# Performance work log

Measured on AMD Instinct MI355X. Metric: run time of the kernel, lower is better.

Reference implementation:

```python
import jax, jax.numpy as jnp
import numpy as np

T, A = 4096, 4          # tokens, atoms per token
N = T * A               # flat atoms
QB, KB = 32, 128        # query block / key window (AF3 atom transformer)
S = N // QB             # number of query subsets
H, DK = 4, 32           # heads, key dim per head
NB = 3                  # transformer blocks
CA, CP, CT = 128, 16, 384

# clipped sliding key window centered on each 32-atom query block
KIDX = jnp.clip(jnp.arange(S)[:, None] * QB - (KB - QB) // 2 + jnp.arange(KB)[None, :], 0, N - 1)

PARAM_SHAPES = [('w_ref_pos', (3, CA)), ('w_ref_mask', (1, CA)), ('w_ref_element', (CA, CA)), ('w_ref_charge', (1, CA)), ('w_ref_atom_name', (256, CA)), ('w_s2p_row', (CA, CP)), ('w_s2p_col', (CA, CP)), ('w_pair_offsets', (3, CP)), ('w_pair_dist', (1, CP)), ('w_pair_mask', (1, CP)), ('w_pair_mlp1', (CP, CP)), ('w_pair_mlp2', (CP, CP)), ('w_pair_mlp3', (CP, CP)), ('w_pair_ln', (CP,)), ('w_pair_logits', (CP, NB * H)), ('aq_lnw', (NB, CA)), ('aq_gw', (NB, CA, CA)), ('aq_gb', (NB, CA)), ('aq_sw', (NB, CA, CA)), ('ak_lnw', (NB, CA)), ('ak_gw', (NB, CA, CA)), ('ak_gb', (NB, CA)), ('ak_sw', (NB, CA, CA)), ('wq', (NB, CA, CA)), ('bq', (NB, CA)), ('wk', (NB, CA, CA)), ('wv', (NB, CA, CA)), ('wg', (NB, CA, CA)), ('azi_w', (NB, CA, CA)), ('azi_cw', (NB, CA, CA)), ('azi_cb', (NB, CA)), ('t_lnw', (NB, CA)), ('t_gw', (NB, CA, CA)), ('t_gb', (NB, CA)), ('t_sw', (NB, CA, CA)), ('glu1', (NB, CA, 2 * CA)), ('glu2', (NB, CA, 2 * CA)), ('t_azi_w', (NB, 2 * CA, CA)), ('t_azi_cw', (NB, CA, CA)), ('t_azi_cb', (NB, CA)), ('w_project', (CA, CT))]


def _ln(x, w=None, eps=1e-5):
    mu = jnp.mean(x, -1, keepdims=True)
    var = jnp.var(x, -1, keepdims=True)
    xn = (x - mu) * jax.lax.rsqrt(var + eps)
    return xn * w if w is not None else xn


def _ada_ln(x, cond, lnw, gw, gb, sw):
    c = _ln(cond, lnw)
    return jax.nn.sigmoid(c @ gw + gb) * _ln(x) + c @ sw


def setup_inputs() -> dict:
    ks = iter(jax.random.split(jax.random.key(0), 64))
    d = {}
    d['positions'] = jax.random.normal(next(ks), (T, A, 3), jnp.float32) * 3.0
    d['mask'] = jnp.ones((T, A), jnp.float32)
    d['element'] = jax.random.randint(next(ks), (T, A), 0, 128, jnp.int32)
    d['charge'] = jax.random.normal(next(ks), (T, A), jnp.float32)
    d['atom_name_chars'] = jax.random.randint(next(ks), (T, A, 4), 0, 64, jnp.int32)
    d['ref_space_uid'] = jax.random.randint(next(ks), (T, A), 0, T, jnp.int32)
    for nm, shp in PARAM_SHAPES:
        if nm.endswith('lnw') or nm == 'w_pair_ln':
            d[nm] = jnp.ones(shp, jnp.float32)
        else:
            d[nm] = jax.random.normal(next(ks), shp, jnp.float32) * 0.02
    return d


def _forward(positions, mask, charge, w_ref_pos, w_ref_mask, w_ref_element, w_ref_charge, w_ref_atom_name, w_s2p_row, w_s2p_col, w_pair_offsets, w_pair_dist, w_pair_mask, w_pair_mlp1, w_pair_mlp2, w_pair_mlp3, w_pair_ln, w_pair_logits, aq_lnw, aq_gw, aq_gb, aq_sw, ak_lnw, ak_gw, ak_gb, ak_sw, wq, bq, wk, wv, wg, azi_w, azi_cw, azi_cb, t_lnw, t_gw, t_gb, t_sw, glu1, glu2, t_azi_w, t_azi_cw, t_azi_cb, w_project, element, atom_name_chars, ref_space_uid):
    dt = positions.dtype
    pos = positions.reshape(N, 3)
    m = mask.reshape(N, 1)
    # per_atom_cond
    el1h = jax.nn.one_hot(element.reshape(N), 128, dtype=dt)
    nm1h = jax.nn.one_hot(atom_name_chars.reshape(N, 4), 64, dtype=dt).reshape(N, 256)
    ch = jnp.arcsinh(charge.reshape(N, 1))
    act = pos @ w_ref_pos + m @ w_ref_mask + el1h @ w_ref_element + ch @ w_ref_charge + nm1h @ w_ref_atom_name
    act = act * m
    qsc = act.reshape(S, QB, CA)  # queries_single_cond
    # pair conditioning
    uid = ref_space_uid.reshape(N)
    q_uid, k_uid = uid.reshape(S, QB), uid[KIDX]
    q_pos, k_pos = pos.reshape(S, QB, 3), pos[KIDX]
    valid = (q_uid[:, :, None] == k_uid[:, None, :]).astype(dt)[..., None]  # [S,QB,KB,1]
    off = q_pos[:, :, None, :] - k_pos[:, None, :, :]  # [S,QB,KB,3]
    pair = (off @ w_pair_offsets) * valid
    sq = jnp.sum(off * off, -1, keepdims=True)
    pair = pair + ((1.0 / (1.0 + sq)) @ w_pair_dist) * valid
    ksc = act[KIDX]  # keys_single_cond [S,KB,CA]
    pair = pair + (jax.nn.relu(qsc) @ w_s2p_row)[:, :, None, :] + (jax.nn.relu(ksc) @ w_s2p_col)[:, None, :, :]
    pair = pair + valid @ w_pair_mask
    t = jax.nn.relu(pair) @ w_pair_mlp1
    t = jax.nn.relu(t) @ w_pair_mlp2
    t = jax.nn.relu(t) @ w_pair_mlp3
    pair = pair + t
    # pair logits for all blocks: [NB, S, H, QB, KB]
    pl = (_ln(pair, w_pair_ln) @ w_pair_logits).reshape(S, QB, KB, NB, H)
    pl = jnp.transpose(pl, (3, 0, 4, 1, 2))
    qact = qsc
    scale = DK ** -0.5
    for i in range(NB):
        kact = qact.reshape(N, CA)[KIDX]
        xq = _ada_ln(qact, qsc, aq_lnw[i], aq_gw[i], aq_gb[i], aq_sw[i])
        xk = _ada_ln(kact, ksc, ak_lnw[i], ak_gw[i], ak_gb[i], ak_sw[i])
        q = (xq @ wq[i] + bq[i]).reshape(S, QB, H, DK)
        k = (xk @ wk[i]).reshape(S, KB, H, DK)
        logits = jnp.einsum('sqhd,skhd->shqk', q * scale, k) + pl[i]
        aw = jax.nn.softmax(logits, axis=-1)
        v = (xk @ wv[i]).reshape(S, KB, H, DK)
        o = jnp.einsum('shqk,skhd->sqhd', aw, v).reshape(S, QB, CA)
        o = o * jax.nn.sigmoid(xq @ wg[i])
        o = (o @ azi_w[i]) * jax.nn.sigmoid(qsc @ azi_cw[i] + azi_cb[i])  # AdaptiveZeroInit
        qact = qact + o
        xt = _ada_ln(qact, qsc, t_lnw[i], t_gw[i], t_gb[i], t_sw[i])
        xt = jax.nn.silu(xt @ glu1[i]) * (xt @ glu2[i])  # SwiGLU
        xt = (xt @ t_azi_w[i]) * jax.nn.sigmoid(qsc @ t_azi_cw[i] + t_azi_cb[i])
        qact = qact + xt
    tok = jax.nn.relu(qact.reshape(T, A, CA) @ w_project)
    mm = mask[..., None]
    token_act = jnp.sum(tok * mm, -2) / jnp.maximum(jnp.sum(mm, -2), 1e-10)
    return token_act, qact, qsc, pair


def reference(positions, mask, element, charge, atom_name_chars, ref_space_uid, w_ref_pos, w_ref_mask, w_ref_element, w_ref_charge, w_ref_atom_name, w_s2p_row, w_s2p_col, w_pair_offsets, w_pair_dist, w_pair_mask, w_pair_mlp1, w_pair_mlp2, w_pair_mlp3, w_pair_ln, w_pair_logits, aq_lnw, aq_gw, aq_gb, aq_sw, ak_lnw, ak_gw, ak_gb, ak_sw, wq, bq, wk, wv, wg, azi_w, azi_cw, azi_cb, t_lnw, t_gw, t_gb, t_sw, glu1, glu2, t_azi_w, t_azi_cw, t_azi_cb, w_project):
    return _forward(positions, mask, charge, w_ref_pos, w_ref_mask, w_ref_element, w_ref_charge, w_ref_atom_name, w_s2p_row, w_s2p_col, w_pair_offsets, w_pair_dist, w_pair_mask, w_pair_mlp1, w_pair_mlp2, w_pair_mlp3, w_pair_ln, w_pair_logits, aq_lnw, aq_gw, aq_gb, aq_sw, ak_lnw, ak_gw, ak_gb, ak_sw, wq, bq, wk, wv, wg, azi_w, azi_cw, azi_cb, t_lnw, t_gw, t_gb, t_sw, glu1, glu2, t_azi_w, t_azi_cw, t_azi_cb, w_project, element, atom_name_chars, ref_space_uid)
```

## Files before the change

kernel.cpp:

```cpp
#include <hip/hip_runtime.h>
#include <math.h>

#define TT 4096
#define AA 4
#define NN 16384
#define QBQ 32
#define KBK 128
#define SS 512
#define HH 4
#define DKD 32
#define CAC 128
#define CPC 16
#define CTC 384

#define EPI_PLAIN 0
#define EPI_SIG   1
#define EPI_RELU  3

typedef __attribute__((ext_vector_type(8))) short bf16x8;
typedef __attribute__((ext_vector_type(4))) short s16x4;
typedef __attribute__((ext_vector_type(4))) float f32x4;

__device__ __forceinline__ float sig_(float x) { return 1.0f / (1.0f + __expf(-x)); }
__device__ __forceinline__ short f2bf(float f) {
    unsigned u = __float_as_uint(f);
    unsigned r = (u + 0x7FFFu + ((u >> 16) & 1u)) >> 16;
    return (short)r;
}
__device__ __forceinline__ float b2f(short s) {
    return __uint_as_float(((unsigned)(unsigned short)s) << 16);
}

struct PEnt { const float* src; const float* rs; short* dst; int K; int NC; };
struct PTab { PEnt e[49]; };

__global__ __launch_bounds__(256) void k_prep(PTab tab)
{
    const PEnt e = tab.e[blockIdx.y];
    const int ntx = e.NC >> 5, nty = e.K >> 5, nt = ntx * nty;
    __shared__ float sm[32][33];
    const int lx = threadIdx.x & 31, ly = threadIdx.x >> 5;
    for (int t = blockIdx.x; t < nt; t += gridDim.x) {
        const int ty = t / ntx, tx = t - ty * ntx;
        #pragma unroll
        for (int j = 0; j < 4; ++j) {
            const int k = ty * 32 + ly + j * 8;
            const int n = tx * 32 + lx;
            float v = e.src[(size_t)k * e.NC + n];
            if (e.rs) v *= e.rs[k];
            sm[ly + j * 8][lx] = v;
        }
        __syncthreads();
        #pragma unroll
        for (int j = 0; j < 4; ++j) {
            const int n = tx * 32 + ly + j * 8;
            const int k = ty * 32 + lx;
            e.dst[(size_t)n * e.K + k] = f2bf(sm[lx][ly + j * 8]);
        }
        __syncthreads();
    }
}

__global__ __launch_bounds__(128) void k_atom_cond(
    const float* __restrict__ pos, const float* __restrict__ msk,
    const int* __restrict__ elem, const float* __restrict__ chg,
    const int* __restrict__ chars,
    const float* __restrict__ w_pos, const float* __restrict__ w_msk,
    const float* __restrict__ w_elem, const float* __restrict__ w_chg,
    const float* __restrict__ w_name,
    const float* __restrict__ w_row, const float* __restrict__ w_col,
    float* __restrict__ qsc, float* __restrict__ qact,
    short* __restrict__ qsc_bf, short* __restrict__ qn_bf,
    float* __restrict__ rq, float* __restrict__ rk)
{
    const int n = blockIdx.x, c = threadIdx.x;
    const float p0 = pos[n*3+0], p1 = pos[n*3+1], p2 = pos[n*3+2];
    const float m = msk[n];
    const int   el = elem[n];
    const float ach = asinhf(chg[n]);
    const int c0 = chars[n*4+0], c1 = chars[n*4+1], c2 = chars[n*4+2], c3 = chars[n*4+3];

    float a = p0*w_pos[c] + p1*w_pos[CAC+c] + p2*w_pos[2*CAC+c]
            + m*w_msk[c] + w_elem[el*CAC+c] + ach*w_chg[c]
            + w_name[(c0      )*CAC+c] + w_name[( 64+c1)*CAC+c]
            + w_name[(128+c2)*CAC+c] + w_name[(192+c3)*CAC+c];
    a *= m;

    const size_t base = (size_t)n*CAC + c;
    qsc[base] = a; qact[base] = a; qsc_bf[base] = f2bf(a);

    __shared__ float red[128];
    __shared__ float sh[128];
    red[c] = a; __syncthreads();
    for (int off = 64; off > 0; off >>= 1) { if (c < off) red[c] += red[c+off]; __syncthreads(); }
    const float mu = red[0] * (1.0f/128.0f);
    __syncthreads();
    const float d = a - mu;
    red[c] = d*d; __syncthreads();
    for (int off = 64; off > 0; off >>= 1) { if (c < off) red[c] += red[c+off]; __syncthreads(); }
    const float var = red[0] * (1.0f/128.0f);
    qn_bf[base] = f2bf(d * rsqrtf(var + 1e-5f));
    __syncthreads();
    sh[c] = fmaxf(a, 0.0f);
    __syncthreads();
    if (c < 32) {
        const float* w = (c < 16) ? w_row : w_col;
        const int cc = c & 15;
        float acc = 0.0f;
        #pragma unroll 8
        for (int r = 0; r < 128; ++r) acc += sh[r] * w[r*CPC + cc];
        if (c < 16) rq[(size_t)n*CPC + cc] = acc;
        else        rk[(size_t)n*CPC + cc] = acc;
    }
}

__global__ __launch_bounds__(256) void k_pair(
    const float* __restrict__ pos, const int* __restrict__ uid,
    const float* __restrict__ rq, const float* __restrict__ rk,
    const float* __restrict__ w_ofs, const float* __restrict__ w_dist,
    const float* __restrict__ w_pm,
    const float* __restrict__ mlp1, const float* __restrict__ mlp2,
    const float* __restrict__ mlp3,
    const float* __restrict__ wln, const float* __restrict__ wpl,
    float* __restrict__ pair, short* __restrict__ plb)
{
    __shared__ float sm1[256], sm2[256], sm3[256], sofs[48], sdist[16], smask[16];
    __shared__ float swln[16], swpl[192];
    const int tid = threadIdx.x;
    sm1[tid] = mlp1[tid]; sm2[tid] = mlp2[tid]; sm3[tid] = mlp3[tid];
    if (tid < 48) sofs[tid] = w_ofs[tid];
    if (tid < 16) { sdist[tid] = w_dist[tid]; smask[tid] = w_pm[tid]; swln[tid] = wln[tid]; }
    if (tid < 192) swpl[tid] = wpl[tid];
    __syncthreads();

    const int gid = blockIdx.x*256 + tid;
    const int s = gid >> 12;
    const int rem = gid & 4095;
    const int q = rem >> 7, kk = rem & 127;
    const int n = s*QBQ + q;
    int kidx = s*QBQ - 48 + kk; kidx = max(0, min(NN-1, kidx));

    const float v = (uid[n] == uid[kidx]) ? 1.0f : 0.0f;
    const float o0 = pos[n*3+0]-pos[kidx*3+0];
    const float o1 = pos[n*3+1]-pos[kidx*3+1];
    const float o2 = pos[n*3+2]-pos[kidx*3+2];
    const float sq = o0*o0 + o1*o1 + o2*o2;
    const float inv = 1.0f/(1.0f + sq);

    const float* rqp = rq + (size_t)n*CPC;
    const float* rkp = rk + (size_t)kidx*CPC;

    float p[16], t1[16], t2[16];
    #pragma unroll
    for (int j = 0; j < 16; ++j)
        p[j] = v*(o0*sofs[j] + o1*sofs[16+j] + o2*sofs[32+j] + inv*sdist[j] + smask[j])
             + rqp[j] + rkp[j];
    #pragma unroll
    for (int j = 0; j < 16; ++j) {
        float acc = 0.0f;
        #pragma unroll
        for (int r = 0; r < 16; ++r) acc += fmaxf(p[r], 0.0f) * sm1[r*16+j];
        t1[j] = acc;
    }
    #pragma unroll
    for (int j = 0; j < 16; ++j) {
        float acc = 0.0f;
        #pragma unroll
        for (int r = 0; r < 16; ++r) acc += fmaxf(t1[r], 0.0f) * sm2[r*16+j];
        t2[j] = acc;
    }
    #pragma unroll
    for (int j = 0; j < 16; ++j) {
        float acc = 0.0f;
        #pragma unroll
        for (int r = 0; r < 16; ++r) acc += fmaxf(t2[r], 0.0f) * sm3[r*16+j];
        t1[j] = p[j] + acc;
    }
    float* op = pair + (size_t)gid*CPC;
    #pragma unroll
    for (int j = 0; j < 4; ++j)
        *(float4*)(op + j*4) = make_float4(t1[j*4], t1[j*4+1], t1[j*4+2], t1[j*4+3]);

    float sm = 0.0f;
    #pragma unroll
    for (int j = 0; j < 16; ++j) sm += t1[j];
    const float mu = sm * (1.0f/16.0f);
    float vq = 0.0f;
    #pragma unroll
    for (int j = 0; j < 16; ++j) { const float dd = t1[j]-mu; vq += dd*dd; }
    const float rs = rsqrtf(vq*(1.0f/16.0f) + 1e-5f);
    float xn[16];
    #pragma unroll
    for (int j = 0; j < 16; ++j) xn[j] = (t1[j]-mu)*rs*swln[j];
    #pragma unroll
    for (int i = 0; i < 3; ++i) {
        #pragma unroll
        for (int h = 0; h < 4; ++h) {
            float acc = 0.0f;
            #pragma unroll
            for (int j = 0; j < 16; ++j) acc += xn[j] * swpl[j*12 + i*4 + h];
            plb[((((size_t)i*SS + s)*HH + h)*QBQ + q)*KBK + kk] = f2bf(acc);
        }
    }
}

__global__ __launch_bounds__(128) void k_resada(
    float* __restrict__ qact, const float* __restrict__ o,
    const short* __restrict__ g,
    const short* __restrict__ G1, const short* __restrict__ S1,
    const short* __restrict__ G2, const short* __restrict__ S2,
    short* __restrict__ x1, short* __restrict__ x2, short* __restrict__ ybf)
{
    const int n = blockIdx.x, c = threadIdx.x;
    const size_t base = (size_t)n*CAC + c;
    float a = qact[base];
    if (o) {
        a += o[base] * b2f(g[base]);
        qact[base] = a;
    }
    if (x1) {
        __shared__ float red[128];
        red[c] = a; __syncthreads();
        for (int off = 64; off > 0; off >>= 1) { if (c < off) red[c] += red[c+off]; __syncthreads(); }
        const float mu = red[0] * (1.0f/128.0f);
        __syncthreads();
        const float d = a - mu;
        red[c] = d*d; __syncthreads();
        for (int off = 64; off > 0; off >>= 1) { if (c < off) red[c] += red[c+off]; __syncthreads(); }
        const float var = red[0] * (1.0f/128.0f);
        const float ln = d * rsqrtf(var + 1e-5f);
        x1[base] = f2bf(b2f(G1[base])*ln + b2f(S1[base]));
        if (x2) x2[base] = f2bf(b2f(G2[base])*ln + b2f(S2[base]));
    }
    if (ybf) ybf[base] = f2bf(a);
}

struct MJob {
    const short* A; const short* Bt; const float* bias;
    float* outF; short* outB;
    int K; int ostride; int epi;
};
struct MJobs { MJob j[8]; };

__global__ __launch_bounds__(256) void k_mm(MJobs jobs)
{
    __shared__ short As[128*64];
    __shared__ short Bs[128*64];
    const MJob J = jobs.j[blockIdx.y];
    const int tid = threadIdx.x;
    const int wave = tid >> 6, lane = tid & 63;
    const int l15 = lane & 15, l4 = lane >> 4;
    const int row0 = blockIdx.x * 128;
    const int K = J.K;

    f32x4 acc[2][8];
    #pragma unroll
    for (int m = 0; m < 2; ++m)
        #pragma unroll
        for (int n = 0; n < 8; ++n) acc[m][n] = (f32x4){0.f,0.f,0.f,0.f};

    for (int k0 = 0; k0 < K; k0 += 64) {
        #pragma unroll
        for (int j = 0; j < 4; ++j) {
            const int u = tid + j*256;
            const int r = u >> 3, ug = u & 7;
            const bf16x8 av = *(const bf16x8*)(J.A + (size_t)(row0 + r)*K + k0 + ug*8);
            *(bf16x8*)&As[r*64 + ((ug ^ (r & 7)) * 8)] = av;
            const bf16x8 bv = *(const bf16x8*)(J.Bt + (size_t)r*K + k0 + ug*8);
            *(bf16x8*)&Bs[r*64 + ((ug ^ (r & 7)) * 8)] = bv;
        }
        __syncthreads();
        #pragma unroll
        for (int ks = 0; ks < 2; ++ks) {
            bf16x8 af[2], bfr[8];
            #pragma unroll
            for (int m = 0; m < 2; ++m) {
                const int r = wave*32 + m*16 + l15;
                af[m] = *(const bf16x8*)&As[r*64 + (((ks*4 + l4) ^ (r & 7)) * 8)];
            }
            #pragma unroll
            for (int n = 0; n < 8; ++n) {
                const int c = n*16 + l15;
                bfr[n] = *(const bf16x8*)&Bs[c*64 + (((ks*4 + l4) ^ (c & 7)) * 8)];
            }
            #pragma unroll
            for (int m = 0; m < 2; ++m)
                #pragma unroll
                for (int n = 0; n < 8; ++n)
                    acc[m][n] = __builtin_amdgcn_mfma_f32_16x16x32_bf16(af[m], bfr[n], acc[m][n], 0, 0, 0);
        }
        __syncthreads();
    }

    float bval[8];
    #pragma unroll
    for (int n = 0; n < 8; ++n) bval[n] = 0.0f;
    if (J.bias) {
        #pragma unroll
        for (int n = 0; n < 8; ++n) bval[n] = J.bias[n*16 + l15];
    }
    const int epi = J.epi;
    #pragma unroll
    for (int m = 0; m < 2; ++m) {
        #pragma unroll
        for (int n = 0; n < 8; ++n) {
            const int col = n*16 + l15;
            #pragma unroll
            for (int reg = 0; reg < 4; ++reg) {
                const int row = row0 + wave*32 + m*16 + l4*4 + reg;
                float v = acc[m][n][reg] + bval[n];
                if (epi == EPI_SIG)  v = sig_(v);
                if (epi == EPI_RELU) v = fmaxf(v, 0.0f);
                if (J.outB) J.outB[(size_t)row*J.ostride + col] = f2bf(v);
                else        J.outF[(size_t)row*J.ostride + col] = v;
            }
        }
    }
}

__global__ __launch_bounds__(256) void k_mm_og(
    const float* __restrict__ Ao, const float* __restrict__ Agt,
    const short* __restrict__ Bt, float* __restrict__ out)
{
    __shared__ short As[128*64];
    __shared__ short Bs[128*64];
    const int tid = threadIdx.x;
    const int wave = tid >> 6, lane = tid & 63;
    const int l15 = lane & 15, l4 = lane >> 4;
    const int row0 = blockIdx.x * 128;

    f32x4 acc[2][8];
    #pragma unroll
    for (int m = 0; m < 2; ++m)
        #pragma unroll
        for (int n = 0; n < 8; ++n) acc[m][n] = (f32x4){0.f,0.f,0.f,0.f};

    for (int k0 = 0; k0 < 128; k0 += 64) {
        #pragma unroll
        for (int j = 0; j < 4; ++j) {
            const int u = tid + j*256;
            const int r = u >> 3, ug = u & 7;
            const size_t ab = (size_t)(row0 + r)*128 + k0 + ug*8;
            const float4 oa = *(const float4*)(Ao + ab);
            const float4 ob = *(const float4*)(Ao + ab + 4);
            const float4 ga = *(const float4*)(Agt + ab);
            const float4 gb = *(const float4*)(Agt + ab + 4);
            bf16x8 av;
            av[0]=f2bf(oa.x*ga.x); av[1]=f2bf(oa.y*ga.y); av[2]=f2bf(oa.z*ga.z); av[3]=f2bf(oa.w*ga.w);
            av[4]=f2bf(ob.x*gb.x); av[5]=f2bf(ob.y*gb.y); av[6]=f2bf(ob.z*gb.z); av[7]=f2bf(ob.w*gb.w);
            *(bf16x8*)&As[r*64 + ((ug ^ (r & 7)) * 8)] = av;
            const bf16x8 bv = *(const bf16x8*)(Bt + (size_t)r*128 + k0 + ug*8);
            *(bf16x8*)&Bs[r*64 + ((ug ^ (r & 7)) * 8)] = bv;
        }
        __syncthreads();
        #pragma unroll
        for (int ks = 0; ks < 2; ++ks) {
            bf16x8 af[2], bfr[8];
            #pragma unroll
            for (int m = 0; m < 2; ++m) {
                const int r = wave*32 + m*16 + l15;
                af[m] = *(const bf16x8*)&As[r*64 + (((ks*4 + l4) ^ (r & 7)) * 8)];
            }
            #pragma unroll
            for (int n = 0; n < 8; ++n) {
                const int c = n*16 + l15;
                bfr[n] = *(const bf16x8*)&Bs[c*64 + (((ks*4 + l4) ^ (c & 7)) * 8)];
            }
            #pragma unroll
            for (int m = 0; m < 2; ++m)
                #pragma unroll
                for (int n = 0; n < 8; ++n)
                    acc[m][n] = __builtin_amdgcn_mfma_f32_16x16x32_bf16(af[m], bfr[n], acc[m][n], 0, 0, 0);
        }
        __syncthreads();
    }

    #pragma unroll
    for (int m = 0; m < 2; ++m)
        #pragma unroll
        for (int n = 0; n < 8; ++n) {
            const int col = n*16 + l15;
            #pragma unroll
            for (int reg = 0; reg < 4; ++reg) {
                const int row = row0 + wave*32 + m*16 + l4*4 + reg;
                out[(size_t)row*128 + col] = acc[m][n][reg];
            }
        }
}

__global__ __launch_bounds__(256) void k_mm_glu(
    const short* __restrict__ A, const short* __restrict__ B1t,
    const short* __restrict__ B2t, short* __restrict__ out)
{
    __shared__ short As[128*64];
    __shared__ short B1s[64*64];
    __shared__ short B2s[64*64];
    const int tid = threadIdx.x;
    const int wave = tid >> 6, lane = tid & 63;
    const int l15 = lane & 15, l4 = lane >> 4;
    const int row0 = blockIdx.x * 128;
    const int col0 = blockIdx.y * 64;

    f32x4 acc1[2][4], acc2[2][4];
    #pragma unroll
    for (int m = 0; m < 2; ++m)
        #pragma unroll
        for (int n = 0; n < 4; ++n) {
            acc1[m][n] = (f32x4){0.f,0.f,0.f,0.f};
            acc2[m][n] = (f32x4){0.f,0.f,0.f,0.f};
        }

    for (int k0 = 0; k0 < 128; k0 += 64) {
        #pragma unroll
        for (int j = 0; j < 4; ++j) {
            const int u = tid + j*256;
            const int r = u >> 3, ug = u & 7;
            const bf16x8 av = *(const bf16x8*)(A + (size_t)(row0 + r)*128 + k0 + ug*8);
            *(bf16x8*)&As[r*64 + ((ug ^ (r & 7)) * 8)] = av;
        }
        #pragma unroll
        for (int j = 0; j < 2; ++j) {
            const int u = tid + j*256;
            const int r = u >> 3, ug = u & 7;
            const bf16x8 b1 = *(const bf16x8*)(B1t + (size_t)(col0 + r)*128 + k0 + ug*8);
            *(bf16x8*)&B1s[r*64 + ((ug ^ (r & 7)) * 8)] = b1;
            const bf16x8 b2 = *(const bf16x8*)(B2t + (size_t)(col0 + r)*128 + k0 + ug*8);
            *(bf16x8*)&B2s[r*64 + ((ug ^ (r & 7)) * 8)] = b2;
        }
        __syncthreads();
        #pragma unroll
        for (int ks = 0; ks < 2; ++ks) {
            bf16x8 af[2], bq1[4], bq2[4];
            #pragma unroll
            for (int m = 0; m < 2; ++m) {
                const int r = wave*32 + m*16 + l15;
                af[m] = *(const bf16x8*)&As[r*64 + (((ks*4 + l4) ^ (r & 7)) * 8)];
            }
            #pragma unroll
            for (int n = 0; n < 4; ++n) {
                const int c = n*16 + l15;
                bq1[n] = *(const bf16x8*)&B1s[c*64 + (((ks*4 + l4) ^ (c & 7)) * 8)];
                bq2[n] = *(const bf16x8*)&B2s[c*64 + (((ks*4 + l4) ^ (c & 7)) * 8)];
            }
            #pragma unroll
            for (int m = 0; m < 2; ++m)
                #pragma unroll
                for (int n = 0; n < 4; ++n) {
                    acc1[m][n] = __builtin_amdgcn_mfma_f32_16x16x32_bf16(af[m], bq1[n], acc1[m][n], 0, 0, 0);
                    acc2[m][n] = __builtin_amdgcn_mfma_f32_16x16x32_bf16(af[m], bq2[n], acc2[m][n], 0, 0, 0);
                }
        }
        __syncthreads();
    }

    #pragma unroll
    for (int m = 0; m < 2; ++m)
        #pragma unroll
        for (int n = 0; n < 4; ++n) {
            const int col = col0 + n*16 + l15;
            #pragma unroll
            for (int reg = 0; reg < 4; ++reg) {
                const int row = row0 + wave*32 + m*16 + l4*4 + reg;
                const float a1 = acc1[m][n][reg];
                const float h = a1 * sig_(a1) * acc2[m][n][reg];
                out[(size_t)row*256 + col] = f2bf(h);
            }
        }
}

__global__ __launch_bounds__(512) void k_attn2(
    const float* __restrict__ qh, const float* __restrict__ kh,
    const float* __restrict__ vh, const short* __restrict__ pls,
    float* __restrict__ oh)
{
    __shared__ float sm_m[256], sm_l[256], sm_acc[256*17];
    const int s = blockIdx.x, tid = threadIdx.x;
    const int kh2 = tid >> 8;
    const int h = (tid >> 6) & 3;
    const int q = (tid >> 1) & 31;
    const int dh = tid & 1;
    const int n0 = s*QBQ;
    const int kbase = n0 - 48 + kh2*64;
    const float SCALE = 0.17677669529663687f;

    float qr[32];
    {
        const float* qp = qh + (size_t)(n0+q)*CAC + h*DKD;
        #pragma unroll
        for (int j = 0; j < 8; ++j) {
            const float4 v4 = *(const float4*)(qp + j*4);
            qr[j*4]=v4.x*SCALE; qr[j*4+1]=v4.y*SCALE; qr[j*4+2]=v4.z*SCALE; qr[j*4+3]=v4.w*SCALE;
        }
    }
    const short* plp = pls + (((size_t)s*HH + h)*QBQ + q)*KBK + kh2*64;

    float m = -1e30f, l = 0.0f;
    float acc[16];
    #pragma unroll
    for (int j = 0; j < 16; ++j) acc[j] = 0.0f;

    for (int kb4 = 0; kb4 < 16; ++kb4) {
        const s16x4 p4 = *(const s16x4*)(plp + kb4*4);
        float pv[4];
        #pragma unroll
        for (int j = 0; j < 4; ++j) pv[j] = b2f(p4[j]);
        #pragma unroll
        for (int j = 0; j < 4; ++j) {
            const int kb = kb4*4 + j;
            int kidx = kbase + kb; kidx = max(0, min(NN-1, kidx));
            const float* kp = kh + (size_t)kidx*CAC + h*DKD;
            float dot = 0.0f;
            #pragma unroll
            for (int jj = 0; jj < 8; ++jj) {
                const float4 kv = *(const float4*)(kp + jj*4);
                dot += qr[jj*4]*kv.x + qr[jj*4+1]*kv.y + qr[jj*4+2]*kv.z + qr[jj*4+3]*kv.w;
            }
            const float sv = dot + pv[j];
            if (sv > m) {
                const float corr = __expf(m - sv);
                l *= corr;
                #pragma unroll
                for (int d = 0; d < 16; ++d) acc[d] *= corr;
                m = sv;
            }
            const float w = __expf(sv - m);
            l += w;
            const float* vp = vh + (size_t)kidx*CAC + h*DKD + dh*16;
            #pragma unroll
            for (int jj = 0; jj < 4; ++jj) {
                const float4 vv = *(const float4*)(vp + jj*4);
                acc[jj*4]   = fmaf(w, vv.x, acc[jj*4]);
                acc[jj*4+1] = fmaf(w, vv.y, acc[jj*4+1]);
                acc[jj*4+2] = fmaf(w, vv.z, acc[jj*4+2]);
                acc[jj*4+3] = fmaf(w, vv.w, acc[jj*4+3]);
            }
        }
    }

    const int part = tid & 255;
    if (kh2 == 1) {
        sm_m[part] = m; sm_l[part] = l;
        #pragma unroll
        for (int j = 0; j < 16; ++j) sm_acc[part*17 + j] = acc[j];
    }
    __syncthreads();
    if (kh2 == 0) {
        const float m2 = sm_m[part], l2 = sm_l[part];
        const float mm = fmaxf(m, m2);
        const float c1 = __expf(m - mm), c2 = __expf(m2 - mm);
        const float inv = 1.0f / (l*c1 + l2*c2);
        float* op = oh + (size_t)(n0+q)*CAC + h*DKD + dh*16;
        #pragma unroll
        for (int jj = 0; jj < 4; ++jj) {
            float o0 = (acc[jj*4  ]*c1 + sm_acc[part*17+jj*4  ]*c2) * inv;
            float o1 = (acc[jj*4+1]*c1 + sm_acc[part*17+jj*4+1]*c2) * inv;
            float o2 = (acc[jj*4+2]*c1 + sm_acc[part*17+jj*4+2]*c2) * inv;
            float o3 = (acc[jj*4+3]*c1 + sm_acc[part*17+jj*4+3]*c2) * inv;
            *(float4*)op = make_float4(o0,o1,o2,o3);
            op += 4;
        }
    }
}

__global__ __launch_bounds__(256) void k_token_reduce(
    const float* __restrict__ tok, const float* __restrict__ msk, float* __restrict__ out)
{
    const int gid = blockIdx.x*256 + threadIdx.x;
    const int t = gid / CTC, c = gid - t*CTC;
    float num = 0.0f, den = 0.0f;
    #pragma unroll
    for (int a = 0; a < AA; ++a) {
        const float mv = msk[t*AA + a];
        num += tok[(size_t)(t*AA+a)*CTC + c] * mv;
        den += mv;
    }
    out[gid] = num / fmaxf(den, 1e-10f);
}

static inline MJob mj(const short* A, const short* Bt, const float* bias,
                      float* outF, short* outB, int K, int ostride, int epi)
{
    MJob j; j.A=A; j.Bt=Bt; j.bias=bias; j.outF=outF; j.outB=outB;
    j.K=K; j.ostride=ostride; j.epi=epi; return j;
}

extern "C" void kernel_launch(void* const* d_in, const int* in_sizes, int n_in,
                              void* d_out, int out_size, void* d_ws, size_t ws_size,
                              hipStream_t stream)
{
    const float* positions = (const float*)d_in[0];
    const float* maskp     = (const float*)d_in[1];
    const int*   element   = (const int*  )d_in[2];
    const float* charge    = (const float*)d_in[3];
    const int*   chars     = (const int*  )d_in[4];
    const int*   uid       = (const int*  )d_in[5];
    const float* w_ref_pos      = (const float*)d_in[6];
    const float* w_ref_mask     = (const float*)d_in[7];
    const float* w_ref_element  = (const float*)d_in[8];
    const float* w_ref_charge   = (const float*)d_in[9];
    const float* w_ref_atom_name= (const float*)d_in[10];
    const float* w_s2p_row      = (const float*)d_in[11];
    const float* w_s2p_col      = (const float*)d_in[12];
    const float* w_pair_offsets = (const float*)d_in[13];
    const float* w_pair_dist    = (const float*)d_in[14];
    const float* w_pair_mask    = (const float*)d_in[15];
    const float* w_pair_mlp1    = (const float*)d_in[16];
    const float* w_pair_mlp2    = (const float*)d_in[17];
    const float* w_pair_mlp3    = (const float*)d_in[18];
    const float* w_pair_ln      = (const float*)d_in[19];
    const float* w_pair_logits  = (const float*)d_in[20];
    const float* aq_lnw = (const float*)d_in[21];
    const float* aq_gw  = (const float*)d_in[22];
    const float* aq_gb  = (const float*)d_in[23];
    const float* aq_sw  = (const float*)d_in[24];
    const float* ak_lnw = (const float*)d_in[25];
    const float* ak_gw  = (const float*)d_in[26];
    const float* ak_gb  = (const float*)d_in[27];
    const float* ak_sw  = (const float*)d_in[28];
    const float* wq     = (const float*)d_in[29];
    const float* bq     = (const float*)d_in[30];
    const float* wk     = (const float*)d_in[31];
    const float* wv     = (const float*)d_in[32];
    const float* wg     = (const float*)d_in[33];
    const float* azi_w  = (const float*)d_in[34];
    const float* azi_cw = (const float*)d_in[35];
    const float* azi_cb = (const float*)d_in[36];
    const float* t_lnw  = (const float*)d_in[37];
    const float* t_gw   = (const float*)d_in[38];
    const float* t_gb   = (const float*)d_in[39];
    const float* t_sw   = (const float*)d_in[40];
    const float* glu1   = (const float*)d_in[41];
    const float* glu2   = (const float*)d_in[42];
    const float* t_azi_w  = (const float*)d_in[43];
    const float* t_azi_cw = (const float*)d_in[44];
    const float* t_azi_cb = (const float*)d_in[45];
    const float* w_project= (const float*)d_in[46];

    float* token_o = (float*)d_out;
    float* qact = token_o + 1572864;
    float* qsc  = token_o + 3670016;
    float* pair = token_o + 5767168;

    char* W = (char*)d_ws;
    short* pl_bf   = (short*)(W);
    short* wbf     = (short*)(W + 50331648);
    short* qn_bf   = (short*)(W + 52428800);
    short* qsc_bf  = (short*)(W + 56623104);
    float* w_op    = (float*)(W + 60817408);
    short* Gq_bf   = (short*)(W + 69206016);
    short* Sq_bf   = (short*)(W + 73400320);
    short* Gk_bf   = (short*)(W + 77594624);
    short* Sk_bf   = (short*)(W + 81788928);
    short* Gt_bf   = (short*)(W + 85983232);
    short* St_bf   = (short*)(W + 90177536);
    short* Ag_bf   = (short*)(W + 94371840);
    short* Tg0_bf  = (short*)(W + 98566144);
    short* xq_bf   = (short*)(W + 102760448);
    short* xk_bf   = (short*)(W + 106954752);
    float* w_q     = (float*)(W + 111149056);
    float* w_k     = (float*)(W + 119537664);
    float* w_v     = (float*)(W + 127926272);
    float* w_g     = (float*)(W + 136314880);
    float* w_o     = (float*)(W + 144703488);
    short* Tg1_bf  = (short*)(W + 153092096);
    short* hs_bf   = (short*)(W + 157286400);
    short* qact_bf = (short*)(W + 165675008);
    float* rq      = (float*)(W + 169869312);
    float* rk      = (float*)(W + 174063616);
    float* tok = w_q;

    (void)in_sizes; (void)n_in; (void)out_size; (void)ws_size;

    const size_t LSTR = 311296;
    const size_t oGQ=0, oSQ=16384, oGK=32768, oSK=49152, oGT=65536, oST=81920,
                 oWQ=98304, oWK=114688, oWV=131072, oWG=147456, oAZ=163840,
                 oACW=180224, oTCW=196608, oG1=212992, oG2=245760, oTAW=278528;
    const size_t oPROJ = 3*LSTR;

    {
        PTab tab{};
        int e = 0;
        for (int i = 0; i < 3; ++i) {
            short* L = wbf + (size_t)i*LSTR;
            const size_t oM = (size_t)i*CAC*CAC, oV = (size_t)i*CAC, oGL = (size_t)i*CAC*2*CAC;
            tab.e[e++] = {aq_gw+oM,  aq_lnw+oV, L+oGQ,  128, 128};
            tab.e[e++] = {aq_sw+oM,  aq_lnw+oV, L+oSQ,  128, 128};
            tab.e[e++] = {ak_gw+oM,  ak_lnw+oV, L+oGK,  128, 128};
            tab.e[e++] = {ak_sw+oM,  ak_lnw+oV, L+oSK,  128, 128};
            tab.e[e++] = {t_gw+oM,   t_lnw+oV,  L+oGT,  128, 128};
            tab.e[e++] = {t_sw+oM,   t_lnw+oV,  L+oST,  128, 128};
            tab.e[e++] = {wq+oM,     nullptr,   L+oWQ,  128, 128};
            tab.e[e++] = {wk+oM,     nullptr,   L+oWK,  128, 128};
            tab.e[e++] = {wv+oM,     nullptr,   L+oWV,  128, 128};
            tab.e[e++] = {wg+oM,     nullptr,   L+oWG,  128, 128};
            tab.e[e++] = {azi_w+oM,  nullptr,   L+oAZ,  128, 128};
            tab.e[e++] = {azi_cw+oM, nullptr,   L+oACW, 128, 128};
            tab.e[e++] = {t_azi_cw+oM,nullptr,  L+oTCW, 128, 128};
            tab.e[e++] = {glu1+oGL,  nullptr,   L+oG1,  128, 256};
            tab.e[e++] = {glu2+oGL,  nullptr,   L+oG2,  128, 256};
            tab.e[e++] = {t_azi_w+oGL,nullptr,  L+oTAW, 256, 128};
        }
        tab.e[e++] = {w_project, nullptr, wbf+oPROJ, 128, 384};
        k_prep<<<dim3(48, 49), 256, 0, stream>>>(tab);
    }

    k_atom_cond<<<NN, 128, 0, stream>>>(positions, maskp, element, charge, chars,
        w_ref_pos, w_ref_mask, w_ref_element, w_ref_charge, w_ref_atom_name,
        w_s2p_row, w_s2p_col, qsc, qact, qsc_bf, qn_bf, rq, rk);

    k_pair<<<(SS*QBQ*KBK)/256, 256, 0, stream>>>(positions, uid, rq, rk,
        w_pair_offsets, w_pair_dist, w_pair_mask, w_pair_mlp1, w_pair_mlp2, w_pair_mlp3,
        w_pair_ln, w_pair_logits, pair, pl_bf);

    for (int i = 0; i < 3; ++i) {
        short* L = wbf + (size_t)i*LSTR;
        const size_t oV = (size_t)i*CAC;
        short* Tg_cur  = (i & 1) ? Tg1_bf : Tg0_bf;
        short* Tg_prev = (i & 1) ? Tg0_bf : Tg1_bf;

        {
            MJobs js{};
            js.j[0] = mj(qn_bf,  L+oGQ,  aq_gb+oV,    nullptr, Gq_bf, 128, 128, EPI_SIG);
            js.j[1] = mj(qn_bf,  L+oSQ,  nullptr,     nullptr, Sq_bf, 128, 128, EPI_PLAIN);
            js.j[2] = mj(qn_bf,  L+oGK,  ak_gb+oV,    nullptr, Gk_bf, 128, 128, EPI_SIG);
            js.j[3] = mj(qn_bf,  L+oSK,  nullptr,     nullptr, Sk_bf, 128, 128, EPI_PLAIN);
            js.j[4] = mj(qn_bf,  L+oGT,  t_gb+oV,     nullptr, Gt_bf, 128, 128, EPI_SIG);
            js.j[5] = mj(qn_bf,  L+oST,  nullptr,     nullptr, St_bf, 128, 128, EPI_PLAIN);
            js.j[6] = mj(qsc_bf, L+oACW, azi_cb+oV,   nullptr, Ag_bf, 128, 128, EPI_SIG);
            js.j[7] = mj(qsc_bf, L+oTCW, t_azi_cb+oV, nullptr, Tg_cur, 128, 128, EPI_SIG);
            k_mm<<<dim3(128, 8), 256, 0, stream>>>(js);
        }
        k_resada<<<NN, 128, 0, stream>>>(qact,
            (i > 0) ? w_op : nullptr, (i > 0) ? Tg_prev : nullptr,
            Gq_bf, Sq_bf, Gk_bf, Sk_bf, xq_bf, xk_bf, nullptr);
        {
            MJobs js{};
            js.j[0] = mj(xq_bf, L+oWQ, bq+oV,   w_q, nullptr, 128, 128, EPI_PLAIN);
            js.j[1] = mj(xk_bf, L+oWK, nullptr, w_k, nullptr, 128, 128, EPI_PLAIN);
            js.j[2] = mj(xk_bf, L+oWV, nullptr, w_v, nullptr, 128, 128, EPI_PLAIN);
            js.j[3] = mj(xq_bf, L+oWG, nullptr, w_g, nullptr, 128, 128, EPI_SIG);
            k_mm<<<dim3(128, 4), 256, 0, stream>>>(js);
        }
        k_attn2<<<SS, 512, 0, stream>>>(w_q, w_k, w_v, pl_bf + (size_t)i*8388608, w_o);
        k_mm_og<<<dim3(128), 256, 0, stream>>>(w_o, w_g, L+oAZ, w_op);
        k_resada<<<NN, 128, 0, stream>>>(qact, w_op, Ag_bf,
            Gt_bf, St_bf, nullptr, nullptr, xq_bf, nullptr, nullptr);
        k_mm_glu<<<dim3(128, 4), 256, 0, stream>>>(xq_bf, L+oG1, L+oG2, hs_bf);
        {
            MJobs js{};
            js.j[0] = mj(hs_bf, L+oTAW, nullptr, w_op, nullptr, 256, 128, EPI_PLAIN);
            k_mm<<<dim3(128, 1), 256, 0, stream>>>(js);
        }
    }
    k_resada<<<NN, 128, 0, stream>>>(qact, w_op, Tg0_bf,
        nullptr, nullptr, nullptr, nullptr, nullptr, nullptr, qact_bf);

    {
        MJobs js{};
        js.j[0] = mj(qact_bf, wbf+oPROJ,       nullptr, tok,     nullptr, 128, 384, EPI_RELU);
        js.j[1] = mj(qact_bf, wbf+oPROJ+16384, nullptr, tok+128, nullptr, 128, 384, EPI_RELU);
        js.j[2] = mj(qact_bf, wbf+oPROJ+32768, nullptr, tok+256, nullptr, 128, 384, EPI_RELU);
        k_mm<<<dim3(128, 3), 256, 0, stream>>>(js);
    }
    k_token_reduce<<<(TT*CTC)/256, 256, 0, stream>>>(tok, maskp, token_o);
}
```

Baseline: 943.6 us.

## Fuse residual-gate and AdaLN into matmul prologues/epilogues, drop k_resada

Removes the standalone residual/AdaLN kernel. Matmul epilogues now apply the gated residual update to qact and emit per-row LayerNorm statistics through shuffle reductions. Downstream matmul prologues rebuild the AdaLN-modulated bf16 operand from fp32 qact, those stats and the G/S tensors. This cuts kernel launches and intermediate bf16 round trips, but operands are recomputed redundantly in each job and variance now uses the single-pass E[x²]-mu² form.

```diff
diff --git a/kernel.cpp b/kernel.cpp
--- a/kernel.cpp
+++ b/kernel.cpp
@@ -13,10 +13,6 @@
 #define CPC 16
 #define CTC 384
 
-#define EPI_PLAIN 0
-#define EPI_SIG   1
-#define EPI_RELU  3
-
 typedef __attribute__((ext_vector_type(8))) short bf16x8;
 typedef __attribute__((ext_vector_type(4))) short s16x4;
 typedef __attribute__((ext_vector_type(4))) float f32x4;
@@ -71,6 +67,7 @@
     const float* __restrict__ w_row, const float* __restrict__ w_col,
     float* __restrict__ qsc, float* __restrict__ qact,
     short* __restrict__ qsc_bf, short* __restrict__ qn_bf,
+    float* __restrict__ stats,
     float* __restrict__ rq, float* __restrict__ rk)
 {
     const int n = blockIdx.x, c = threadIdx.x;
@@ -99,7 +96,9 @@
     red[c] = d*d; __syncthreads();
     for (int off = 64; off > 0; off >>= 1) { if (c < off) red[c] += red[c+off]; __syncthreads(); }
     const float var = red[0] * (1.0f/128.0f);
-    qn_bf[base] = f2bf(d * rsqrtf(var + 1e-5f));
+    const float rs = rsqrtf(var + 1e-5f);
+    qn_bf[base] = f2bf(d * rs);
+    if (c == 0) { stats[2*n] = mu; stats[2*n+1] = rs; }
     __syncthreads();
     sh[c] = fmaxf(a, 0.0f);
     __syncthreads();
@@ -204,49 +203,21 @@
     }
 }
 
-__global__ __launch_bounds__(128) void k_resada(
-    float* __restrict__ qact, const float* __restrict__ o,
-    const short* __restrict__ g,
-    const short* __restrict__ G1, const short* __restrict__ S1,
-    const short* __restrict__ G2, const short* __restrict__ S2,
-    short* __restrict__ x1, short* __restrict__ x2, short* __restrict__ ybf)
-{
-    const int n = blockIdx.x, c = threadIdx.x;
-    const size_t base = (size_t)n*CAC + c;
-    float a = qact[base];
-    if (o) {
-        a += o[base] * b2f(g[base]);
-        qact[base] = a;
-    }
-    if (x1) {
-        __shared__ float red[128];
-        red[c] = a; __syncthreads();
-        for (int off = 64; off > 0; off >>= 1) { if (c < off) red[c] += red[c+off]; __syncthreads(); }
-        const float mu = red[0] * (1.0f/128.0f);
-        __syncthreads();
-        const float d = a - mu;
-        red[c] = d*d; __syncthreads();
-        for (int off = 64; off > 0; off >>= 1) { if (c < off) red[c] += red[c+off]; __syncthreads(); }
-        const float var = red[0] * (1.0f/128.0f);
-        const float ln = d * rsqrtf(var + 1e-5f);
-        x1[base] = f2bf(b2f(G1[base])*ln + b2f(S1[base]));
-        if (x2) x2[base] = f2bf(b2f(G2[base])*ln + b2f(S2[base]));
-    }
-    if (ybf) ybf[base] = f2bf(a);
-}
-
-struct MJob {
-    const short* A; const short* Bt; const float* bias;
+struct FJob {
+    const void* A; const void* A2;
+    const float* stats; const short* G; const short* S;
+    const short* Bt; const float* bias;
     float* outF; short* outB;
-    int K; int ostride; int epi;
+    const short* gate; float* resid; float* ostats;
+    int K; int ostride; int amode; int emode;
 };
-struct MJobs { MJob j[8]; };
-
-__global__ __launch_bounds__(256) void k_mm(MJobs jobs)
+struct FJobs { FJob j[8]; };
+
+__global__ __launch_bounds__(256) void k_mmf(FJobs jobs)
 {
     __shared__ short As[128*64];
     __shared__ short Bs[128*64];
-    const MJob J = jobs.j[blockIdx.y];
+    const FJob J = jobs.j[blockIdx.y];
     const int tid = threadIdx.x;
     const int wave = tid >> 6, lane = tid & 63;
     const int l15 = lane & 15, l4 = lane >> 4;
@@ -264,7 +235,40 @@
         for (int j = 0; j < 4; ++j) {
             const int u = tid + j*256;
             const int r = u >> 3, ug = u & 7;
-            const bf16x8 av = *(const bf16x8*)(J.A + (size_t)(row0 + r)*K + k0 + ug*8);
+            const int row = row0 + r;
+            const size_t ao = (size_t)row*K + k0 + ug*8;
+            bf16x8 av;
+            if (J.amode == 0) {
+                av = *(const bf16x8*)((const short*)J.A + ao);
+            } else if (J.amode == 1) {
+                const float* Af = (const float*)J.A;
+                const float4 a0 = *(const float4*)(Af + ao);
+                const float4 a1 = *(const float4*)(Af + ao + 4);
+                const float mu = J.stats[2*row], rs = J.stats[2*row+1];
+                const s16x4 g0 = *(const s16x4*)(J.G + ao), g1 = *(const s16x4*)(J.G + ao + 4);
+                const s16x4 s0 = *(const s16x4*)(J.S + ao), s1 = *(const s16x4*)(J.S + ao + 4);
+                const float x[8] = {a0.x,a0.y,a0.z,a0.w,a1.x,a1.y,a1.z,a1.w};
+                #pragma unroll
+                for (int t = 0; t < 4; ++t) {
+                    av[t]   = f2bf(b2f(g0[t])*((x[t]  -mu)*rs) + b2f(s0[t]));
+                    av[t+4] = f2bf(b2f(g1[t])*((x[t+4]-mu)*rs) + b2f(s1[t]));
+                }
+            } else if (J.amode == 2) {
+                const float* Ao = (const float*)J.A;
+                const float* Ag = (const float*)J.A2;
+                const float4 oa = *(const float4*)(Ao + ao);
+                const float4 ob = *(const float4*)(Ao + ao + 4);
+                const float4 ga = *(const float4*)(Ag + ao);
+                const float4 gb = *(const float4*)(Ag + ao + 4);
+                av[0]=f2bf(oa.x*ga.x); av[1]=f2bf(oa.y*ga.y); av[2]=f2bf(oa.z*ga.z); av[3]=f2bf(oa.w*ga.w);
+                av[4]=f2bf(ob.x*gb.x); av[5]=f2bf(ob.y*gb.y); av[6]=f2bf(ob.z*gb.z); av[7]=f2bf(ob.w*gb.w);
+            } else {
+                const float* Af = (const float*)J.A;
+                const float4 a0 = *(const float4*)(Af + ao);
+                const float4 a1 = *(const float4*)(Af + ao + 4);
+                av[0]=f2bf(a0.x); av[1]=f2bf(a0.y); av[2]=f2bf(a0.z); av[3]=f2bf(a0.w);
+                av[4]=f2bf(a1.x); av[5]=f2bf(a1.y); av[6]=f2bf(a1.z); av[7]=f2bf(a1.w);
+            }
             *(bf16x8*)&As[r*64 + ((ug ^ (r & 7)) * 8)] = av;
             const bf16x8 bv = *(const bf16x8*)(J.Bt + (size_t)r*K + k0 + ug*8);
             *(bf16x8*)&Bs[r*64 + ((ug ^ (r & 7)) * 8)] = bv;
@@ -292,105 +296,67 @@
         __syncthreads();
     }
 
-    float bval[8];
-    #pragma unroll
-    for (int n = 0; n < 8; ++n) bval[n] = 0.0f;
-    if (J.bias) {
-        #pragma unroll
-        for (int n = 0; n < 8; ++n) bval[n] = J.bias[n*16 + l15];
-    }
-    const int epi = J.epi;
-    #pragma unroll
-    for (int m = 0; m < 2; ++m) {
-        #pragma unroll
-        for (int n = 0; n < 8; ++n) {
-            const int col = n*16 + l15;
+    if (J.emode == 3) {
+        #pragma unroll
+        for (int m = 0; m < 2; ++m) {
             #pragma unroll
             for (int reg = 0; reg < 4; ++reg) {
                 const int row = row0 + wave*32 + m*16 + l4*4 + reg;
-                float v = acc[m][n][reg] + bval[n];
-                if (epi == EPI_SIG)  v = sig_(v);
-                if (epi == EPI_RELU) v = fmaxf(v, 0.0f);
-                if (J.outB) J.outB[(size_t)row*J.ostride + col] = f2bf(v);
-                else        J.outF[(size_t)row*J.ostride + col] = v;
-            }
-        }
-    }
-}
-
-__global__ __launch_bounds__(256) void k_mm_og(
-    const float* __restrict__ Ao, const float* __restrict__ Agt,
-    const short* __restrict__ Bt, float* __restrict__ out)
-{
-    __shared__ short As[128*64];
-    __shared__ short Bs[128*64];
-    const int tid = threadIdx.x;
-    const int wave = tid >> 6, lane = tid & 63;
-    const int l15 = lane & 15, l4 = lane >> 4;
-    const int row0 = blockIdx.x * 128;
-
-    f32x4 acc[2][8];
-    #pragma unroll
-    for (int m = 0; m < 2; ++m)
-        #pragma unroll
-        for (int n = 0; n < 8; ++n) acc[m][n] = (f32x4){0.f,0.f,0.f,0.f};
-
-    for (int k0 = 0; k0 < 128; k0 += 64) {
-        #pragma unroll
-        for (int j = 0; j < 4; ++j) {
-            const int u = tid + j*256;
-            const int r = u >> 3, ug = u & 7;
-            const size_t ab = (size_t)(row0 + r)*128 + k0 + ug*8;
-            const float4 oa = *(const float4*)(Ao + ab);
-            const float4 ob = *(const float4*)(Ao + ab + 4);
-            const float4 ga = *(const float4*)(Agt + ab);
-            const float4 gb = *(const float4*)(Agt + ab + 4);
-            bf16x8 av;
-            av[0]=f2bf(oa.x*ga.x); av[1]=f2bf(oa.y*ga.y); av[2]=f2bf(oa.z*ga.z); av[3]=f2bf(oa.w*ga.w);
-            av[4]=f2bf(ob.x*gb.x); av[5]=f2bf(ob.y*gb.y); av[6]=f2bf(ob.z*gb.z); av[7]=f2bf(ob.w*gb.w);
-            *(bf16x8*)&As[r*64 + ((ug ^ (r & 7)) * 8)] = av;
-            const bf16x8 bv = *(const bf16x8*)(Bt + (size_t)r*128 + k0 + ug*8);
-            *(bf16x8*)&Bs[r*64 + ((ug ^ (r & 7)) * 8)] = bv;
-        }
-        __syncthreads();
-        #pragma unroll
-        for (int ks = 0; ks < 2; ++ks) {
-            bf16x8 af[2], bfr[8];
-            #pragma unroll
-            for (int m = 0; m < 2; ++m) {
-                const int r = wave*32 + m*16 + l15;
-                af[m] = *(const bf16x8*)&As[r*64 + (((ks*4 + l4) ^ (r & 7)) * 8)];
-            }
+                float s = 0.0f, q = 0.0f;
+                #pragma unroll
+                for (int n = 0; n < 8; ++n) {
+                    const int col = n*16 + l15;
+                    const size_t off = (size_t)row*CAC + col;
+                    const float v = J.resid[off] + acc[m][n][reg] * b2f(J.gate[off]);
+                    J.resid[off] = v;
+                    s += v; q += v*v;
+                }
+                #pragma unroll
+                for (int msk = 1; msk < 16; msk <<= 1) {
+                    s += __shfl_xor(s, msk, 64);
+                    q += __shfl_xor(q, msk, 64);
+                }
+                if (l15 == 0) {
+                    const float mu = s * (1.0f/128.0f);
+                    const float var = q * (1.0f/128.0f) - mu*mu;
+                    J.ostats[2*row]   = mu;
+                    J.ostats[2*row+1] = rsqrtf(var + 1e-5f);
+                }
+            }
+        }
+    } else {
+        float bval[8];
+        #pragma unroll
+        for (int n = 0; n < 8; ++n) bval[n] = 0.0f;
+        if (J.bias) {
+            #pragma unroll
+            for (int n = 0; n < 8; ++n) bval[n] = J.bias[n*16 + l15];
+        }
+        const int epi = J.emode;
+        #pragma unroll
+        for (int m = 0; m < 2; ++m) {
             #pragma unroll
             for (int n = 0; n < 8; ++n) {
-                const int c = n*16 + l15;
-                bfr[n] = *(const bf16x8*)&Bs[c*64 + (((ks*4 + l4) ^ (c & 7)) * 8)];
-            }
-            #pragma unroll
-            for (int m = 0; m < 2; ++m)
+                const int col = n*16 + l15;
                 #pragma unroll
-                for (int n = 0; n < 8; ++n)
-                    acc[m][n] = __builtin_amdgcn_mfma_f32_16x16x32_bf16(af[m], bfr[n], acc[m][n], 0, 0, 0);
-        }
-        __syncthreads();
-    }
-
-    #pragma unroll
-    for (int m = 0; m < 2; ++m)
-        #pragma unroll
-        for (int n = 0; n < 8; ++n) {
-            const int col = n*16 + l15;
-            #pragma unroll
-            for (int reg = 0; reg < 4; ++reg) {
-                const int row = row0 + wave*32 + m*16 + l4*4 + reg;
-                out[(size_t)row*128 + col] = acc[m][n][reg];
-            }
-        }
+                for (int reg = 0; reg < 4; ++reg) {
+                    const int row = row0 + wave*32 + m*16 + l4*4 + reg;
+                    float v = acc[m][n][reg] + bval[n];
+                    if (epi == 1) v = sig_(v);
+                    if (epi == 2) v = fmaxf(v, 0.0f);
+                    if (J.outB) J.outB[(size_t)row*J.ostride + col] = f2bf(v);
+                    else        J.outF[(size_t)row*J.ostride + col] = v;
+                }
+            }
+        }
+    }
 }
 
 __global__ __launch_bounds__(256) void k_mm_glu(
-    const short* __restrict__ A, const short* __restrict__ B1t,
-    const short* __restrict__ B2t, short* __restrict__ out)
+    const float* __restrict__ qact, const float* __restrict__ stats,
+    const short* __restrict__ Gt, const short* __restrict__ St,
+    const short* __restrict__ B1t, const short* __restrict__ B2t,
+    short* __restrict__ out)
 {
     __shared__ short As[128*64];
     __shared__ short B1s[64*64];
@@ -415,7 +381,20 @@
         for (int j = 0; j < 4; ++j) {
             const int u = tid + j*256;
             const int r = u >> 3, ug = u & 7;
-            const bf16x8 av = *(const bf16x8*)(A + (size_t)(row0 + r)*128 + k0 + ug*8);
+            const int row = row0 + r;
+            const size_t ao = (size_t)row*CAC + k0 + ug*8;
+            const float4 a0 = *(const float4*)(qact + ao);
+            const float4 a1 = *(const float4*)(qact + ao + 4);
+            const float mu = stats[2*row], rs = stats[2*row+1];
+            const s16x4 g0 = *(const s16x4*)(Gt + ao), g1 = *(const s16x4*)(Gt + ao + 4);
+            const s16x4 s0 = *(const s16x4*)(St + ao), s1 = *(const s16x4*)(St + ao + 4);
+            const float x[8] = {a0.x,a0.y,a0.z,a0.w,a1.x,a1.y,a1.z,a1.w};
+            bf16x8 av;
+            #pragma unroll
+            for (int t = 0; t < 4; ++t) {
+                av[t]   = f2bf(b2f(g0[t])*((x[t]  -mu)*rs) + b2f(s0[t]));
+                av[t+4] = f2bf(b2f(g1[t])*((x[t+4]-mu)*rs) + b2f(s1[t]));
+            }
             *(bf16x8*)&As[r*64 + ((ug ^ (r & 7)) * 8)] = av;
         }
         #pragma unroll
@@ -577,12 +556,7 @@
     out[gid] = num / fmaxf(den, 1e-10f);
 }
 
-static inline MJob mj(const short* A, const short* Bt, const float* bias,
-                      float* outF, short* outB, int K, int ostride, int epi)
-{
-    MJob j; j.A=A; j.Bt=Bt; j.bias=bias; j.outF=outF; j.outB=outB;
-    j.K=K; j.ostride=ostride; j.epi=epi; return j;
-}
+static inline FJob fj0() { FJob j{}; return j; }
 
 extern "C" void kernel_launch(void* const* d_in, const int* in_sizes, int n_in,
                               void* d_out, int out_size, void* d_ws, size_t ws_size,
@@ -646,27 +620,23 @@
     short* wbf     = (short*)(W + 50331648);
     short* qn_bf   = (short*)(W + 52428800);
     short* qsc_bf  = (short*)(W + 56623104);
-    float* w_op    = (float*)(W + 60817408);
-    short* Gq_bf   = (short*)(W + 69206016);
-    short* Sq_bf   = (short*)(W + 73400320);
-    short* Gk_bf   = (short*)(W + 77594624);
-    short* Sk_bf   = (short*)(W + 81788928);
-    short* Gt_bf   = (short*)(W + 85983232);
-    short* St_bf   = (short*)(W + 90177536);
-    short* Ag_bf   = (short*)(W + 94371840);
-    short* Tg0_bf  = (short*)(W + 98566144);
-    short* xq_bf   = (short*)(W + 102760448);
-    short* xk_bf   = (short*)(W + 106954752);
-    float* w_q     = (float*)(W + 111149056);
-    float* w_k     = (float*)(W + 119537664);
-    float* w_v     = (float*)(W + 127926272);
-    float* w_g     = (float*)(W + 136314880);
-    float* w_o     = (float*)(W + 144703488);
-    short* Tg1_bf  = (short*)(W + 153092096);
-    short* hs_bf   = (short*)(W + 157286400);
-    short* qact_bf = (short*)(W + 165675008);
-    float* rq      = (float*)(W + 169869312);
-    float* rk      = (float*)(W + 174063616);
+    float* stats   = (float*)(W + 60817408);
+    short* Gq_bf   = (short*)(W + 60948480);
+    short* Sq_bf   = (short*)(W + 65142784);
+    short* Gk_bf   = (short*)(W + 69337088);
+    short* Sk_bf   = (short*)(W + 73531392);
+    short* Gt_bf   = (short*)(W + 77725696);
+    short* St_bf   = (short*)(W + 81920000);
+    short* Ag_bf   = (short*)(W + 86114304);
+    short* Tg_bf   = (short*)(W + 90308608);
+    float* w_q     = (float*)(W + 94502912);
+    float* w_k     = (float*)(W + 102891520);
+    float* w_v     = (float*)(W + 111280128);
+    float* w_g     = (float*)(W + 119668736);
+    float* w_o     = (float*)(W + 128057344);
+    short* hs_bf   = (short*)(W + 136445952);
+    float* rq      = (float*)(W + 144834560);
+    float* rk      = (float*)(W + 145883136);
     float* tok = w_q;
 
     (void)in_sizes; (void)n_in; (void)out_size; (void)ws_size;
@@ -706,7 +676,7 @@
 
     k_atom_cond<<<NN, 128, 0, stream>>>(positions, maskp, element, charge, chars,
         w_ref_pos, w_ref_mask, w_ref_element, w_ref_charge, w_ref_atom_name,
-        w_s2p_row, w_s2p_col, qsc, qact, qsc_bf, qn_bf, rq, rk);
+        w_s2p_row, w_s2p_col, qsc, qact, qsc_bf, qn_bf, stats, rq, rk);
 
     k_pair<<<(SS*QBQ*KBK)/256, 256, 0, stream>>>(positions, uid, rq, rk,
         w_pair_offsets, w_pair_dist, w_pair_mask, w_pair_mlp1, w_pair_mlp2, w_pair_mlp3,
@@ -715,52 +685,69 @@
     for (int i = 0; i < 3; ++i) {
         short* L = wbf + (size_t)i*LSTR;
         const size_t oV = (size_t)i*CAC;
-        short* Tg_cur  = (i & 1) ? Tg1_bf : Tg0_bf;
-        short* Tg_prev = (i & 1) ? Tg0_bf : Tg1_bf;
 
         {
-            MJobs js{};
-            js.j[0] = mj(qn_bf,  L+oGQ,  aq_gb+oV,    nullptr, Gq_bf, 128, 128, EPI_SIG);
-            js.j[1] = mj(qn_bf,  L+oSQ,  nullptr,     nullptr, Sq_bf, 128, 128, EPI_PLAIN);
-            js.j[2] = mj(qn_bf,  L+oGK,  ak_gb+oV,    nullptr, Gk_bf, 128, 128, EPI_SIG);
-            js.j[3] = mj(qn_bf,  L+oSK,  nullptr,     nullptr, Sk_bf, 128, 128, EPI_PLAIN);
-            js.j[4] = mj(qn_bf,  L+oGT,  t_gb+oV,     nullptr, Gt_bf, 128, 128, EPI_SIG);
-            js.j[5] = mj(qn_bf,  L+oST,  nullptr,     nullptr, St_bf, 128, 128, EPI_PLAIN);
-            js.j[6] = mj(qsc_bf, L+oACW, azi_cb+oV,   nullptr, Ag_bf, 128, 128, EPI_SIG);
-            js.j[7] = mj(qsc_bf, L+oTCW, t_azi_cb+oV, nullptr, Tg_cur, 128, 128, EPI_SIG);
-            k_mm<<<dim3(128, 8), 256, 0, stream>>>(js);
-        }
-        k_resada<<<NN, 128, 0, stream>>>(qact,
-            (i > 0) ? w_op : nullptr, (i > 0) ? Tg_prev : nullptr,
-            Gq_bf, Sq_bf, Gk_bf, Sk_bf, xq_bf, xk_bf, nullptr);
+            FJobs js{};
+            struct { const short* A; const short* Bt; const float* bias; short* out; int em; } cfg[8] = {
+                {qn_bf,  L+oGQ,  aq_gb+oV,    Gq_bf, 1}, {qn_bf,  L+oSQ,  nullptr, Sq_bf, 0},
+                {qn_bf,  L+oGK,  ak_gb+oV,    Gk_bf, 1}, {qn_bf,  L+oSK,  nullptr, Sk_bf, 0},
+                {qn_bf,  L+oGT,  t_gb+oV,     Gt_bf, 1}, {qn_bf,  L+oST,  nullptr, St_bf, 0},
+                {qsc_bf, L+oACW, azi_cb+oV,   Ag_bf, 1}, {qsc_bf, L+oTCW, t_azi_cb+oV, Tg_bf, 1}};
+            for (int jn = 0; jn < 8; ++jn) {
+                FJob j = fj0();
+                j.A = cfg[jn].A; j.Bt = cfg[jn].Bt; j.bias = cfg[jn].bias;
+                j.outB = cfg[jn].out; j.K = 128; j.ostride = 128;
+                j.amode = 0; j.emode = cfg[jn].em;
+                js.j[jn] = j;
+            }
+            k_mmf<<<dim3(128, 8), 256, 0, stream>>>(js);
+        }
         {
-            MJobs js{};
-            js.j[0] = mj(xq_bf, L+oWQ, bq+oV,   w_q, nullptr, 128, 128, EPI_PLAIN);
-            js.j[1] = mj(xk_bf, L+oWK, nullptr, w_k, nullptr, 128, 128, EPI_PLAIN);
-            js.j[2] = mj(xk_bf, L+oWV, nullptr, w_v, nullptr, 128, 128, EPI_PLAIN);
-            js.j[3] = mj(xq_bf, L+oWG, nullptr, w_g, nullptr, 128, 128, EPI_SIG);
-            k_mm<<<dim3(128, 4), 256, 0, stream>>>(js);
+            FJobs js{};
+            struct { const short* G; const short* S; const short* Bt; const float* bias; float* out; int em; } cfg[4] = {
+                {Gq_bf, Sq_bf, L+oWQ, bq+oV,   w_q, 0}, {Gk_bf, Sk_bf, L+oWK, nullptr, w_k, 0},
+                {Gk_bf, Sk_bf, L+oWV, nullptr, w_v, 0}, {Gq_bf, Sq_bf, L+oWG, nullptr, w_g, 1}};
+            for (int jn = 0; jn < 4; ++jn) {
+                FJob j = fj0();
+                j.A = qact; j.stats = stats; j.G = cfg[jn].G; j.S = cfg[jn].S;
+                j.Bt = cfg[jn].Bt; j.bias = cfg[jn].bias; j.outF = cfg[jn].out;
+                j.K = 128; j.ostride = 128; j.amode = 1; j.emode = cfg[jn].em;
+                js.j[jn] = j;
+            }
+            k_mmf<<<dim3(128, 4), 256, 0, stream>>>(js);
         }
         k_attn2<<<SS, 512, 0, stream>>>(w_q, w_k, w_v, pl_bf + (size_t)i*8388608, w_o);
-        k_mm_og<<<dim3(128), 256, 0, stream>>>(w_o, w_g, L+oAZ, w_op);
-        k_resada<<<NN, 128, 0, stream>>>(qact, w_op, Ag_bf,
-            Gt_bf, St_bf, nullptr, nullptr, xq_bf, nullptr, nullptr);
-        k_mm_glu<<<dim3(128, 4), 256, 0, stream>>>(xq_bf, L+oG1, L+oG2, hs_bf);
         {
-            MJobs js{};
-            js.j[0] = mj(hs_bf, L+oTAW, nullptr, w_op, nullptr, 256, 128, EPI_PLAIN);
-            k_mm<<<dim3(128, 1), 256, 0, stream>>>(js);
-        }
-    }
-    k_resada<<<NN, 128, 0, stream>>>(qact, w_op, Tg0_bf,
-        nullptr, nullptr, nullptr, nullptr, nullptr, nullptr, qact_bf);
+            FJobs js{};
+            FJob j = fj0();
+            j.A = w_o; j.A2 = w_g; j.Bt = L+oAZ;
+            j.gate = Ag_bf; j.resid = qact; j.ostats = stats;
+            j.K = 128; j.ostride = 128; j.amode = 2; j.emode = 3;
+            js.j[0] = j;
+            k_mmf<<<dim3(128, 1), 256, 0, stream>>>(js);
+        }
+        k_mm_glu<<<dim3(128, 4), 256, 0, stream>>>(qact, stats, Gt_bf, St_bf, L+oG1, L+oG2, hs_bf);
+        {
+            FJobs js{};
+            FJob j = fj0();
+            j.A = hs_bf; j.Bt = L+oTAW;
+            j.gate = Tg_bf; j.resid = qact; j.ostats = stats;
+            j.K = 256; j.ostride = 128; j.amode = 0; j.emode = 3;
+            js.j[0] = j;
+            k_mmf<<<dim3(128, 1), 256, 0, stream>>>(js);
+        }
+    }
 
     {
-        MJobs js{};
-        js.j[0] = mj(qact_bf, wbf+oPROJ,       nullptr, tok,     nullptr, 128, 384, EPI_RELU);
-        js.j[1] = mj(qact_bf, wbf+oPROJ+16384, nullptr, tok+128, nullptr, 128, 384, EPI_RELU);
-        js.j[2] = mj(qact_bf, wbf+oPROJ+32768, nullptr, tok+256, nullptr, 128, 384, EPI_RELU);
-        k_mm<<<dim3(128, 3), 256, 0, stream>>>(js);
+        FJobs js{};
+        for (int c = 0; c < 3; ++c) {
+            FJob j = fj0();
+            j.A = qact; j.Bt = wbf + oPROJ + (size_t)c*16384;
+            j.outF = tok + c*128;
+            j.K = 128; j.ostride = 384; j.amode = 3; j.emode = 2;
+            js.j[c] = j;
+        }
+        k_mmf<<<dim3(128, 3), 256, 0, stream>>>(js);
     }
     k_token_reduce<<<(TT*CTC)/256, 256, 0, stream>>>(tok, maskp, token_o);
 }
```

After: 933.9 us. About the same (-1.0%).
